# Performance work log

Hardware: AMD Instinct MI355X
Metric: run time of the kernel (lower is better)

Reference implementation:

```python
import jax, jax.numpy as jnp
import numpy as np


def setup_inputs() -> dict:
    key = jax.random.key(0)
    kq, kk, kv = jax.random.split(key, 3)
    n, m, d, v = 4096, 4096, 1024, 1024
    Q = jax.random.normal(kq, (n, d), dtype=jnp.float32)
    K = jax.random.normal(kk, (m, d), dtype=jnp.float32)
    V = jax.random.normal(kv, (m, v), dtype=jnp.float32)
    return {"Q": Q, "K": K, "V": V}


def reference(Q, K, V):
    d = K.shape[-1]
    scale = d ** (-0.5)
    logits = jnp.matmul(Q, K.T)                      # [n, m]
    # Faithful to source: softmax over dim=1 (keys), THEN scaled by d**-0.5
    scores = jax.nn.softmax(logits, axis=1) * scale  # [n, m]
    return jnp.matmul(scores, V)                     # [n, v]
```

## Files before the change

kernel.cpp:

```cpp
#include <hip/hip_runtime.h>
#include <hip/hip_bf16.h>

typedef _Float16 f16x8 __attribute__((ext_vector_type(8)));
typedef _Float16 f16x4 __attribute__((ext_vector_type(4)));
typedef float f32x4 __attribute__((ext_vector_type(4)));

__device__ __forceinline__ void async_ld16(_Float16* lds, const _Float16* g) {
    __builtin_amdgcn_global_load_lds(
        (const __attribute__((address_space(1))) void*)g,
        (__attribute__((address_space(3))) void*)lds, 16, 0, 0);
}

__global__ __launch_bounds__(256) void gemm_bt(
    const _Float16* __restrict__ A,
    const _Float16* __restrict__ B,
    float* __restrict__ C,
    int M, int N, int K, int Ks)
{
    __shared__ _Float16 At[2][128 * 32];
    __shared__ _Float16 Bt[2][128 * 32];

    const int tid  = threadIdx.x;
    const int wave = tid >> 6;
    const int lane = tid & 63;

    int gx = gridDim.x, gy = gridDim.y;
    int bx = blockIdx.x, by = blockIdx.y;
    if (((gx & 7) == 0) && ((gy & 7) == 0)) {
        const int bid    = bx + gx * by;
        const int ntx    = gx >> 3;
        const int sid    = bid >> 6;
        const int within = bid & 63;
        const int sx = sid % ntx;
        const int sy = sid / ntx;
        bx = (sx << 3) + (within & 7);
        by = (sy << 3) + (within >> 3);
    }
    const int row0 = by * 128;
    const int col0 = bx * 128;

    const int wr = (wave >> 1) * 64;
    const int wc = (wave & 1) * 64;
    const int quad = lane >> 4;
    const int l16  = lane & 15;

    f32x4 acc[4][4] = {};

    const int srow  = lane >> 2;
    const int skoff = (lane & 3) * 8;
    const size_t K64 = (size_t)64 * K;

    const _Float16* Ab = A + (size_t)row0 * K + (size_t)blockIdx.z * Ks;
    const _Float16* Bb = B + (size_t)col0 * K + (size_t)blockIdx.z * Ks;
    float* Cb = C + (size_t)blockIdx.z * M * N;

    const _Float16* pa = Ab + (size_t)(wave * 16 + srow) * K + skoff;
    const _Float16* pb = Bb + (size_t)(wave * 16 + srow) * K + skoff;

    async_ld16(At[0] + wave * 512,       pa);
    async_ld16(At[0] + (wave + 4) * 512, pa + K64);
    async_ld16(Bt[0] + wave * 512,       pb);
    async_ld16(Bt[0] + (wave + 4) * 512, pb + K64);
    __syncthreads();

    int cur = 0;
    for (int k0 = 0; k0 < Ks; k0 += 32) {
        const int nxt = cur ^ 1;
        if (k0 + 32 < Ks) {
            const _Float16* qa = pa + k0 + 32;
            const _Float16* qb = pb + k0 + 32;
            async_ld16(At[nxt] + wave * 512,       qa);
            async_ld16(At[nxt] + (wave + 4) * 512, qa + K64);
            async_ld16(Bt[nxt] + wave * 512,       qb);
            async_ld16(Bt[nxt] + (wave + 4) * 512, qb + K64);
        }

        f16x8 af[4], bf[4];
        #pragma unroll
        for (int r = 0; r < 4; ++r)
            af[r] = *(const f16x8*)&At[cur][(wr + r * 16 + l16) * 32 + quad * 8];
        #pragma unroll
        for (int c = 0; c < 4; ++c)
            bf[c] = *(const f16x8*)&Bt[cur][(wc + c * 16 + l16) * 32 + quad * 8];

        #pragma unroll
        for (int r = 0; r < 4; ++r)
            #pragma unroll
            for (int c = 0; c < 4; ++c)
                acc[r][c] = __builtin_amdgcn_mfma_f32_16x16x32_f16(af[r], bf[c], acc[r][c], 0, 0, 0);

        __syncthreads();
        cur = nxt;
    }

    #pragma unroll
    for (int r = 0; r < 4; ++r) {
        const int growb = row0 + wr + r * 16 + quad * 4;
        #pragma unroll
        for (int c = 0; c < 4; ++c) {
            const int gcol = col0 + wc + c * 16 + l16;
            #pragma unroll
            for (int i = 0; i < 4; ++i)
                Cb[(size_t)(growb + i) * N + gcol] = acc[r][c][i];
        }
    }
}

__global__ __launch_bounds__(256) void softmax_rows(
    const float* __restrict__ S, _Float16* __restrict__ P, float scale)
{
    __shared__ float red[4];
    const int row = blockIdx.x;
    const int tid = threadIdx.x;
    const int wave = tid >> 6;
    const float4* Sr = (const float4*)(S + (size_t)row * 4096);

    float4 x[4];
    #pragma unroll
    for (int i = 0; i < 4; ++i) x[i] = Sr[tid + i * 256];

    float mx = -3.402823466e+38f;
    #pragma unroll
    for (int i = 0; i < 4; ++i)
        mx = fmaxf(mx, fmaxf(fmaxf(x[i].x, x[i].y), fmaxf(x[i].z, x[i].w)));
    #pragma unroll
    for (int off = 32; off > 0; off >>= 1) mx = fmaxf(mx, __shfl_down(mx, off));
    if ((tid & 63) == 0) red[wave] = mx;
    __syncthreads();
    mx = fmaxf(fmaxf(red[0], red[1]), fmaxf(red[2], red[3]));
    __syncthreads();

    float sum = 0.0f;
    #pragma unroll
    for (int i = 0; i < 4; ++i) {
        x[i].x = __expf(x[i].x - mx);
        x[i].y = __expf(x[i].y - mx);
        x[i].z = __expf(x[i].z - mx);
        x[i].w = __expf(x[i].w - mx);
        sum += x[i].x + x[i].y + x[i].z + x[i].w;
    }
    #pragma unroll
    for (int off = 32; off > 0; off >>= 1) sum += __shfl_down(sum, off);
    if ((tid & 63) == 0) red[wave] = sum;
    __syncthreads();
    sum = red[0] + red[1] + red[2] + red[3];

    const float inv = scale / sum;
    f16x4* Pr = (f16x4*)(P + (size_t)row * 4096);
    #pragma unroll
    for (int i = 0; i < 4; ++i) {
        f16x4 h;
        h.x = (_Float16)(x[i].x * inv);
        h.y = (_Float16)(x[i].y * inv);
        h.z = (_Float16)(x[i].z * inv);
        h.w = (_Float16)(x[i].w * inv);
        Pr[tid + i * 256] = h;
    }
}

__global__ __launch_bounds__(256) void cvt2_f32_f16(
    const float4* __restrict__ a, f16x4* __restrict__ da, int n4a,
    const float4* __restrict__ b, f16x4* __restrict__ db, int n4b)
{
    int i = blockIdx.x * 256 + threadIdx.x;
    const int stride = gridDim.x * 256;
    const int tot = n4a + n4b;
    for (; i < tot; i += stride) {
        const float4* s = (i < n4a) ? (a + i) : (b + (i - n4a));
        f16x4* d = (i < n4a) ? (da + i) : (db + (i - n4a));
        float4 v = *s;
        f16x4 h;
        h.x = (_Float16)v.x; h.y = (_Float16)v.y;
        h.z = (_Float16)v.z; h.w = (_Float16)v.w;
        *d = h;
    }
}

__global__ __launch_bounds__(256) void transpose_cvt(
    const float* __restrict__ V, _Float16* __restrict__ Vt, int rows, int cols)
{
    __shared__ float tile[32][33];
    const int c0 = blockIdx.x * 32;
    const int r0 = blockIdx.y * 32;
    const int tx = threadIdx.x & 31;
    const int ty = threadIdx.x >> 5;
    #pragma unroll
    for (int i = 0; i < 4; ++i)
        tile[ty * 4 + i][tx] = V[(size_t)(r0 + ty * 4 + i) * cols + c0 + tx];
    __syncthreads();
    #pragma unroll
    for (int i = 0; i < 4; ++i)
        Vt[(size_t)(c0 + ty * 4 + i) * rows + r0 + tx] = (_Float16)tile[tx][ty * 4 + i];
}

__global__ __launch_bounds__(256) void reduce2(
    const float4* __restrict__ a, const float4* __restrict__ b,
    float4* __restrict__ o, int n4)
{
    int i = blockIdx.x * 256 + threadIdx.x;
    const int stride = gridDim.x * 256;
    for (; i < n4; i += stride) {
        float4 u = a[i], v = b[i];
        float4 w;
        w.x = u.x + v.x; w.y = u.y + v.y; w.z = u.z + v.z; w.w = u.w + v.w;
        o[i] = w;
    }
}

extern "C" void kernel_launch(void* const* d_in, const int* in_sizes, int n_in,
                              void* d_out, int out_size, void* d_ws, size_t ws_size,
                              hipStream_t stream) {
    const float* Q = (const float*)d_in[0];
    const float* K = (const float*)d_in[1];
    const float* V = (const float*)d_in[2];
    float* out = (float*)d_out;

    const int n = 4096, m = 4096, d = 1024, vdim = 1024;
    const float scale = 0.03125f;

    char* w = (char*)d_ws;
    _Float16* Qh = (_Float16*)w;
    _Float16* Kh = (_Float16*)(w + (8u << 20));
    _Float16* Vt = (_Float16*)(w + (16u << 20));
    char* rest = w + (24u << 20);
    size_t avail = ws_size > (24u << 20) ? ws_size - (24u << 20) : 0;

    int nc = 128;
    if      ((size_t)4096 * m * 6 <= avail) nc = 4096;
    else if ((size_t)2048 * m * 6 <= avail) nc = 2048;
    else if ((size_t)1024 * m * 6 <= avail) nc = 1024;
    else if ((size_t)512  * m * 6 <= avail) nc = 512;
    else if ((size_t)256  * m * 6 <= avail) nc = 256;

    float*    S = (float*)rest;
    _Float16* P = (_Float16*)(rest + (size_t)nc * m * 4);
    float* part = S;

    cvt2_f32_f16<<<dim3(2048), dim3(256), 0, stream>>>(
        (const float4*)Q, (f16x4*)Qh, n * d / 4,
        (const float4*)K, (f16x4*)Kh, m * d / 4);
    transpose_cvt<<<dim3(vdim / 32, m / 32), dim3(256), 0, stream>>>(V, Vt, m, vdim);

    for (int r0 = 0; r0 < n; r0 += nc) {
        gemm_bt<<<dim3(m / 128, nc / 128, 1), dim3(256), 0, stream>>>(
            Qh + (size_t)r0 * d, Kh, S, nc, m, d, d);
        softmax_rows<<<dim3(nc), dim3(256), 0, stream>>>(S, P, scale);
        gemm_bt<<<dim3(vdim / 128, nc / 128, 2), dim3(256), 0, stream>>>(
            P, Vt, part, nc, vdim, m, m / 2);
        reduce2<<<dim3(1024), dim3(256), 0, stream>>>(
            (const float4*)part, (const float4*)(part + (size_t)nc * vdim),
            (float4*)(out + (size_t)r0 * vdim), nc * vdim / 4);
    }
}
```

Measured before the change: 212.9 us.

## Add 256x256-tile GEMM with XCD-aware block remap and 4-way split-K

Measured after the change: 220.7 us. +3.6%, slower.

```diff
diff --git a/kernel.cpp b/kernel.cpp
--- a/kernel.cpp
+++ b/kernel.cpp
@@ -9,6 +9,113 @@
     __builtin_amdgcn_global_load_lds(
         (const __attribute__((address_space(1))) void*)g,
         (__attribute__((address_space(3))) void*)lds, 16, 0, 0);
+}
+
+__global__ __launch_bounds__(512, 2) void gemm_bt256(
+    const _Float16* __restrict__ A,
+    const _Float16* __restrict__ B,
+    float* __restrict__ C,
+    int M, int N, int K, int Ks)
+{
+    __shared__ _Float16 Asm[2][256 * 32];
+    __shared__ _Float16 Bsm[2][256 * 32];
+
+    const int tid  = threadIdx.x;
+    const int w    = tid >> 6;
+    const int lane = tid & 63;
+    const int l16  = lane & 15;
+    const int quad = lane >> 4;
+    const int wm   = w >> 2;
+    const int wn   = w & 3;
+
+    const int gx = gridDim.x, gy = gridDim.y;
+    const int total = gx * gy * (int)gridDim.z;
+    int lid = (int)blockIdx.x + gx * ((int)blockIdx.y + gy * (int)blockIdx.z);
+    {
+        const int q = total >> 3, r = total & 7;
+        const int xcd = lid & 7, i = lid >> 3;
+        lid = (xcd < r ? xcd * (q + 1) : r * (q + 1) + (xcd - r) * q) + i;
+    }
+    const int bx = lid % gx;
+    const int by = (lid / gx) % gy;
+    const int bz = lid / (gx * gy);
+
+    const int row0 = by * 256;
+    const int col0 = bx * 256;
+
+    const _Float16* Ab = A + (size_t)row0 * K + (size_t)bz * Ks;
+    const _Float16* Bb = B + (size_t)col0 * K + (size_t)bz * Ks;
+
+    const int srow = lane >> 2;
+    const int sch  = (lane & 3) * 8;
+    const _Float16* pa = Ab + (size_t)(w * 32 + srow) * K + sch;
+    const _Float16* pb = Bb + (size_t)(w * 32 + srow) * K + sch;
+    const size_t r16 = (size_t)16 * K;
+
+    f32x4 acc[8][4] = {};
+    const int NT = Ks >> 5;
+
+    {
+        _Float16* as = &Asm[0][0] + w * 1024;
+        _Float16* bs = &Bsm[0][0] + w * 1024;
+        async_ld16(as,       pa);
+        async_ld16(as + 512, pa + r16);
+        async_ld16(bs,       pb);
+        async_ld16(bs + 512, pb + r16);
+    }
+    __syncthreads();
+
+    const int aoff = (wm * 16 + l16) * 32 + quad * 8;
+    const int boff = (wn * 16 + l16) * 32 + quad * 8;
+
+    for (int t = 0; t < NT; ++t) {
+        const int buf = t & 1;
+
+        if (t + 1 < NT) {
+            const int kc = (t + 1) * 32;
+            _Float16* as = &Asm[buf ^ 1][0] + w * 1024;
+            _Float16* bs = &Bsm[buf ^ 1][0] + w * 1024;
+            async_ld16(as,       pa + kc);
+            async_ld16(as + 512, pa + kc + r16);
+            async_ld16(bs,       pb + kc);
+            async_ld16(bs + 512, pb + kc + r16);
+        }
+
+        const _Float16* abuf = &Asm[buf][0];
+        const _Float16* bbuf = &Bsm[buf][0];
+
+        f16x8 af[8], bf[4];
+        #pragma unroll
+        for (int i = 0; i < 8; ++i)
+            af[i] = *(const f16x8*)(abuf + (i >> 2) * 4096 + (i & 3) * 1024 + aoff);
+        #pragma unroll
+        for (int j = 0; j < 4; ++j)
+            bf[j] = *(const f16x8*)(bbuf + (j >> 1) * 4096 + (j & 1) * 2048 + boff);
+
+        #pragma unroll
+        for (int i = 0; i < 8; ++i)
+            #pragma unroll
+            for (int j = 0; j < 4; ++j)
+                acc[i][j] = __builtin_amdgcn_mfma_f32_16x16x32_f16(af[i], bf[j], acc[i][j], 0, 0, 0);
+
+        __syncthreads();
+    }
+
+    float* Cb = C + (size_t)bz * ((size_t)M * N);
+    #pragma unroll
+    for (int i = 0; i < 8; ++i) {
+        const int ms = i >> 2, m = i & 3;
+        const int gr = row0 + ms * 128 + m * 32 + wm * 16 + quad * 4;
+        #pragma unroll
+        for (int j = 0; j < 4; ++j) {
+            const int ns = j >> 1, nn = j & 1;
+            const int gc = col0 + ns * 128 + nn * 64 + wn * 16 + l16;
+            const f32x4 v = acc[i][j];
+            #pragma unroll
+            for (int e = 0; e < 4; ++e)
+                Cb[(size_t)(gr + e) * N + gc] = v[e];
+        }
+    }
 }
 
 __global__ __launch_bounds__(256) void gemm_bt(
@@ -207,6 +314,24 @@
     }
 }
 
+__global__ __launch_bounds__(256) void reduce4(
+    const float4* __restrict__ a, const float4* __restrict__ b,
+    const float4* __restrict__ c, const float4* __restrict__ d,
+    float4* __restrict__ o, int n4)
+{
+    int i = blockIdx.x * 256 + threadIdx.x;
+    const int stride = gridDim.x * 256;
+    for (; i < n4; i += stride) {
+        float4 u = a[i], v = b[i], x = c[i], y = d[i];
+        float4 w;
+        w.x = (u.x + v.x) + (x.x + y.x);
+        w.y = (u.y + v.y) + (x.y + y.y);
+        w.z = (u.z + v.z) + (x.z + y.z);
+        w.w = (u.w + v.w) + (x.w + y.w);
+        o[i] = w;
+    }
+}
+
 extern "C" void kernel_launch(void* const* d_in, const int* in_sizes, int n_in,
                               void* d_out, int out_size, void* d_ws, size_t ws_size,
                               hipStream_t stream) {
@@ -241,14 +366,30 @@
         (const float4*)K, (f16x4*)Kh, m * d / 4);
     transpose_cvt<<<dim3(vdim / 32, m / 32), dim3(256), 0, stream>>>(V, Vt, m, vdim);
 
-    for (int r0 = 0; r0 < n; r0 += nc) {
-        gemm_bt<<<dim3(m / 128, nc / 128, 1), dim3(256), 0, stream>>>(
-            Qh + (size_t)r0 * d, Kh, S, nc, m, d, d);
-        softmax_rows<<<dim3(nc), dim3(256), 0, stream>>>(S, P, scale);
-        gemm_bt<<<dim3(vdim / 128, nc / 128, 2), dim3(256), 0, stream>>>(
-            P, Vt, part, nc, vdim, m, m / 2);
-        reduce2<<<dim3(1024), dim3(256), 0, stream>>>(
-            (const float4*)part, (const float4*)(part + (size_t)nc * vdim),
-            (float4*)(out + (size_t)r0 * vdim), nc * vdim / 4);
-    }
-}
+    if (nc >= 256) {
+        for (int r0 = 0; r0 < n; r0 += nc) {
+            gemm_bt256<<<dim3(m / 256, nc / 256, 1), dim3(512), 0, stream>>>(
+                Qh + (size_t)r0 * d, Kh, S, nc, m, d, d);
+            softmax_rows<<<dim3(nc), dim3(256), 0, stream>>>(S, P, scale);
+            gemm_bt256<<<dim3(vdim / 256, nc / 256, 4), dim3(512), 0, stream>>>(
+                P, Vt, part, nc, vdim, m, m / 4);
+            reduce4<<<dim3(1024), dim3(256), 0, stream>>>(
+                (const float4*)part,
+                (const float4*)(part + (size_t)nc * vdim),
+                (const float4*)(part + (size_t)2 * nc * vdim),
+                (const float4*)(part + (size_t)3 * nc * vdim),
+                (float4*)(out + (size_t)r0 * vdim), nc * vdim / 4);
+        }
+    } else {
+        for (int r0 = 0; r0 < n; r0 += nc) {
+            gemm_bt<<<dim3(m / 128, nc / 128, 1), dim3(256), 0, stream>>>(
+                Qh + (size_t)r0 * d, Kh, S, nc, m, d, d);
+            softmax_rows<<<dim3(nc), dim3(256), 0, stream>>>(S, P, scale);
+            gemm_bt<<<dim3(vdim / 128, nc / 128, 2), dim3(256), 0, stream>>>(
+                P, Vt, part, nc, vdim, m, m / 2);
+            reduce2<<<dim3(1024), dim3(256), 0, stream>>>(
+                (const float4*)part, (const float4*)(part + (size_t)nc * vdim),
+                (float4*)(out + (size_t)r0 * vdim), nc * vdim / 4);
+        }
+    }
+}
```
